# Kernel optimization log

Hardware: AMD Instinct MI355X
Metric: run time of the kernel (lower is better)

The kernel has to match this reference:

```python
import jax, jax.numpy as jnp
import numpy as np


def _conv1d(x, w, b):
    # x: [N, C_in, L], w: [C_out, C_in, K], padding=1 (SAME for K=3)
    y = jax.lax.conv_general_dilated(
        x, w, window_strides=(1,), padding=[(1, 1)],
        dimension_numbers=('NCH', 'OIH', 'NCH'))
    return y + b[None, :, None]


def _pharse_shift(I, r):
    # Faithful vectorized form of the original scalar loop:
    #   New[i, 0, j] = I[i, j % r, j // r];  all other output channels stay zero.
    a, b, c = I.shape
    row0 = jnp.transpose(I[:, :r, :], (0, 2, 1)).reshape(a, c * r)  # interleave channels
    New = jnp.zeros((a, b // r, c * r), dtype=I.dtype)
    return New.at[:, 0, :].set(row0)


def setup_inputs() -> dict:
    key = jax.random.key(0)
    k1, k2, k3, k4, k5 = jax.random.split(key, 5)
    B, C, L = 32, 64, 16384
    x = jax.random.normal(k1, (B, C, L), dtype=jnp.float32)
    # Conv1d(channels, channels, 3) params, PyTorch-style uniform init scale
    s1 = 1.0 / np.sqrt(C * 3)
    w1 = jax.random.uniform(k2, (C, C, 3), minval=-s1, maxval=s1, dtype=jnp.float32)
    b1 = jax.random.uniform(k3, (C,), minval=-s1, maxval=s1, dtype=jnp.float32)
    # Conv1d(channels, 4, 3) params (up_block22)
    w2 = jax.random.uniform(k4, (4, C, 3), minval=-s1, maxval=s1, dtype=jnp.float32)
    b2 = jax.random.uniform(k5, (4,), minval=-s1, maxval=s1, dtype=jnp.float32)
    return {"x": x, "w1": w1, "b1": b1, "w2": w2, "b2": b2, "sc": 4}


def reference(x, w1, b1, w2, b2, sc):
    assert sc in (2, 4)
    h = jax.nn.relu(_conv1d(x, w1, b1))   # up_block1: Conv1d(C,C,3)+ReLU
    h = jax.nn.relu(_conv1d(h, w2, b2))   # up_block22: Conv1d(C,4,3)+ReLU  [B,4,L]
    return _pharse_shift(h, sc)           # [B, 4//sc, L*sc]
```

## Files before the change

### kernel.cpp

```cpp
#include <hip/hip_runtime.h>


#define CC 64
#define LL 16384
#define NBATCH 32
#define TL 128
#define XROWS 146
#define PITCH 128

typedef short short8 __attribute__((ext_vector_type(8)));
typedef float f32x4 __attribute__((ext_vector_type(4)));

__device__ __forceinline__ unsigned short f2bf(float f) {
    unsigned u = __builtin_bit_cast(unsigned, f);
    u = (u + 0x7FFFu + ((u >> 16) & 1u)) >> 16;
    return (unsigned short)u;
}

__global__ void repack_weights(const float* __restrict__ w1,
                               const float* __restrict__ w2,
                               unsigned short* __restrict__ wp) {
    int i = blockIdx.x * 256 + threadIdx.x;
    if (i < 12288) {
        int kk = i >> 12;
        int rem = i & 4095;
        int co = rem >> 6;
        int ci = rem & 63;
        wp[i] = f2bf(w1[(co * 64 + ci) * 3 + kk]);
    }
    if (i < 3072) {
        int kk = i >> 10;
        int rem = i & 1023;
        int oc = rem >> 6;
        int ci = rem & 63;
        float v = (oc < 4) ? w2[(oc * 64 + ci) * 3 + kk] : 0.0f;
        wp[12288 + i] = f2bf(v);
    }
}

__global__ __launch_bounds__(256, 4)
void fused_upsample_mfma(const float* __restrict__ x,
                         const float* __restrict__ b1,
                         const float* __restrict__ b2,
                         const unsigned short* __restrict__ wp,
                         float* __restrict__ out) {
    __shared__ __align__(16) char lds[(148 + 144) * PITCH];
    char* const xs = lds;
    char* const hs = lds + 148 * PITCH;

    const int t    = blockIdx.x;
    const int bb   = blockIdx.y;
    const int tid  = threadIdx.x;
    const int lane = tid & 63;
    const int wave = tid >> 6;
    const int lr   = lane & 15;
    const int lg   = lane >> 4;

    {
        const int c   = tid & 15;
        const int cg  = tid >> 4;
        const int ci0 = cg * 4;
        const long xbase = (long)(bb * CC + ci0) * LL;
        #pragma unroll
        for (int it = 0; it < 10; ++it) {
            int row = it * 16 + c;
            if (row < XROWS) {
                int gx = t * TL - 2 + row;
                bool ok = (unsigned)gx < (unsigned)LL;
                float v0 = ok ? x[xbase + gx]          : 0.f;
                float v1 = ok ? x[xbase + LL + gx]     : 0.f;
                float v2 = ok ? x[xbase + 2 * LL + gx] : 0.f;
                float v3 = ok ? x[xbase + 3 * LL + gx] : 0.f;
                unsigned lo = (unsigned)f2bf(v0) | ((unsigned)f2bf(v1) << 16);
                unsigned hi = (unsigned)f2bf(v2) | ((unsigned)f2bf(v3) << 16);
                int byte = (row * PITCH + ci0 * 2) ^ ((row & 7) << 4);
                *(uint2*)(xs + byte) = make_uint2(lo, hi);
            }
        }
    }
    __syncthreads();

    {
        short8 A1[3][2];
        #pragma unroll
        for (int k = 0; k < 3; ++k)
            #pragma unroll
            for (int kc = 0; kc < 2; ++kc)
                A1[k][kc] = *(const short8*)(wp + ((k * 64 + wave * 16 + lr) * 64 + kc * 32 + lg * 8));

        const f32x4 bias1 = *(const f32x4*)(b1 + wave * 16 + lg * 4);

        #pragma unroll 1
        for (int i = 0; i < 9; ++i) {
            f32x4 acc = {0.f, 0.f, 0.f, 0.f};
            #pragma unroll
            for (int k = 0; k < 3; ++k) {
                int row = 16 * i + lr + k;
                #pragma unroll
                for (int kc = 0; kc < 2; ++kc) {
                    int byte = (row * PITCH + kc * 64 + lg * 16) ^ ((row & 7) << 4);
                    short8 Bf = *(const short8*)(xs + byte);
                    acc = __builtin_amdgcn_mfma_f32_16x16x32_bf16(A1[k][kc], Bf, acc, 0, 0, 0);
                }
            }
            int p  = 16 * i - 1 + lr;
            int hp = t * TL + p;
            bool inr = (unsigned)hp < (unsigned)LL;
            float r0 = inr ? fmaxf(acc[0] + bias1[0], 0.f) : 0.f;
            float r1 = inr ? fmaxf(acc[1] + bias1[1], 0.f) : 0.f;
            float r2 = inr ? fmaxf(acc[2] + bias1[2], 0.f) : 0.f;
            float r3 = inr ? fmaxf(acc[3] + bias1[3], 0.f) : 0.f;
            unsigned lo = (unsigned)f2bf(r0) | ((unsigned)f2bf(r1) << 16);
            unsigned hi = (unsigned)f2bf(r2) | ((unsigned)f2bf(r3) << 16);
            int hrow = 16 * i + lr;
            int byte = (hrow * PITCH + wave * 32 + lg * 8) ^ ((hrow & 7) << 4);
            *(uint2*)(hs + byte) = make_uint2(lo, hi);
        }
    }
    __syncthreads();

    {
        short8 A2[3][2];
        #pragma unroll
        for (int k = 0; k < 3; ++k)
            #pragma unroll
            for (int kc = 0; kc < 2; ++kc)
                A2[k][kc] = *(const short8*)(wp + 12288 + ((k * 16 + lr) * 64 + kc * 32 + lg * 8));

        const f32x4 bias2 = *(const f32x4*)(b2);

        #pragma unroll
        for (int s = 0; s < 2; ++s) {
            int p0 = 16 * (wave * 2 + s);
            f32x4 acc = {0.f, 0.f, 0.f, 0.f};
            #pragma unroll
            for (int k = 0; k < 3; ++k) {
                int row = p0 + lr + k;
                #pragma unroll
                for (int kc = 0; kc < 2; ++kc) {
                    int byte = (row * PITCH + kc * 64 + lg * 16) ^ ((row & 7) << 4);
                    short8 Bf = *(const short8*)(hs + byte);
                    acc = __builtin_amdgcn_mfma_f32_16x16x32_bf16(A2[k][kc], Bf, acc, 0, 0, 0);
                }
            }
            if (lane < 16) {
                f32x4 o;
                o[0] = fmaxf(acc[0] + bias2[0], 0.f);
                o[1] = fmaxf(acc[1] + bias2[1], 0.f);
                o[2] = fmaxf(acc[2] + bias2[2], 0.f);
                o[3] = fmaxf(acc[3] + bias2[3], 0.f);
                *(f32x4*)(out + (long)bb * (LL * 4) + (t * TL + p0 + lane) * 4) = o;
            }
        }
    }
}

extern "C" void kernel_launch(void* const* d_in, const int* in_sizes, int n_in,
                              void* d_out, int out_size, void* d_ws, size_t ws_size,
                              hipStream_t stream) {
    const float* x  = (const float*)d_in[0];
    const float* w1 = (const float*)d_in[1];
    const float* b1 = (const float*)d_in[2];
    const float* w2 = (const float*)d_in[3];
    const float* b2 = (const float*)d_in[4];
    float* out = (float*)d_out;
    unsigned short* wp = (unsigned short*)d_ws;

    repack_weights<<<48, 256, 0, stream>>>(w1, w2, wp);
    dim3 grid(LL / TL, NBATCH);
    fused_upsample_mfma<<<grid, 256, 0, stream>>>(x, b1, b2, wp, out);
}
```

Baseline: 64.11 us.

## Process four tiles per block with register-prefetched input and reorganized wave work split

Each block now loops over four consecutive L-tiles. It prefetches the next tile's x values into registers while the current tile's MFMA convolutions run, then writes them to LDS after the first barrier. Waves are re-split so each wave computes two output-channel groups over half the position chunks, sharing B fragments across two MFMAs. Biases are folded into the accumulator init, and bf16 conversion now uses the library intrinsic. This amortizes weight loads and hides global-load latency, at the cost of more registers (launch bounds lowered to 3), an extra barrier per tile, and a grid four times smaller.

```diff
diff --git a/kernel.cpp b/kernel.cpp
--- a/kernel.cpp
+++ b/kernel.cpp
@@ -1,20 +1,22 @@
 #include <hip/hip_runtime.h>
+#include <hip/hip_bf16.h>
 
 
 #define CC 64
 #define LL 16384
 #define NBATCH 32
 #define TL 128
+#define NT 4
 #define XROWS 146
 #define PITCH 128
 
 typedef short short8 __attribute__((ext_vector_type(8)));
 typedef float f32x4 __attribute__((ext_vector_type(4)));
 
-__device__ __forceinline__ unsigned short f2bf(float f) {
-    unsigned u = __builtin_bit_cast(unsigned, f);
-    u = (u + 0x7FFFu + ((u >> 16) & 1u)) >> 16;
-    return (unsigned short)u;
+__device__ __forceinline__ unsigned pk2(float a, float b) {
+    unsigned short lo = __builtin_bit_cast(unsigned short, __float2bfloat16(a));
+    unsigned short hi = __builtin_bit_cast(unsigned short, __float2bfloat16(b));
+    return (unsigned)lo | ((unsigned)hi << 16);
 }
 
 __global__ void repack_weights(const float* __restrict__ w1,
@@ -26,7 +28,7 @@
         int rem = i & 4095;
         int co = rem >> 6;
         int ci = rem & 63;
-        wp[i] = f2bf(w1[(co * 64 + ci) * 3 + kk]);
+        wp[i] = __builtin_bit_cast(unsigned short, __float2bfloat16(w1[(co * 64 + ci) * 3 + kk]));
     }
     if (i < 3072) {
         int kk = i >> 10;
@@ -34,105 +36,130 @@
         int oc = rem >> 6;
         int ci = rem & 63;
         float v = (oc < 4) ? w2[(oc * 64 + ci) * 3 + kk] : 0.0f;
-        wp[12288 + i] = f2bf(v);
-    }
-}
-
-__global__ __launch_bounds__(256, 4)
+        wp[12288 + i] = __builtin_bit_cast(unsigned short, __float2bfloat16(v));
+    }
+}
+
+__global__ __launch_bounds__(256, 3)
 void fused_upsample_mfma(const float* __restrict__ x,
                          const float* __restrict__ b1,
                          const float* __restrict__ b2,
                          const unsigned short* __restrict__ wp,
                          float* __restrict__ out) {
-    __shared__ __align__(16) char lds[(148 + 144) * PITCH];
+    __shared__ __align__(16) char lds[(XROWS + 144) * PITCH];
     char* const xs = lds;
-    char* const hs = lds + 148 * PITCH;
-
-    const int t    = blockIdx.x;
+    char* const hs = lds + XROWS * PITCH;
+
+    const int t0   = blockIdx.x * NT;
     const int bb   = blockIdx.y;
     const int tid  = threadIdx.x;
     const int lane = tid & 63;
     const int wave = tid >> 6;
     const int lr   = lane & 15;
     const int lg   = lane >> 4;
-
-    {
-        const int c   = tid & 15;
-        const int cg  = tid >> 4;
-        const int ci0 = cg * 4;
-        const long xbase = (long)(bb * CC + ci0) * LL;
-        #pragma unroll
-        for (int it = 0; it < 10; ++it) {
-            int row = it * 16 + c;
-            if (row < XROWS) {
-                int gx = t * TL - 2 + row;
-                bool ok = (unsigned)gx < (unsigned)LL;
-                float v0 = ok ? x[xbase + gx]          : 0.f;
-                float v1 = ok ? x[xbase + LL + gx]     : 0.f;
-                float v2 = ok ? x[xbase + 2 * LL + gx] : 0.f;
-                float v3 = ok ? x[xbase + 3 * LL + gx] : 0.f;
-                unsigned lo = (unsigned)f2bf(v0) | ((unsigned)f2bf(v1) << 16);
-                unsigned hi = (unsigned)f2bf(v2) | ((unsigned)f2bf(v3) << 16);
-                int byte = (row * PITCH + ci0 * 2) ^ ((row & 7) << 4);
-                *(uint2*)(xs + byte) = make_uint2(lo, hi);
-            }
-        }
-    }
-    __syncthreads();
-
-    {
-        short8 A1[3][2];
+    const int c2   = wave & 1;
+    const int ph   = wave >> 1;
+
+    short8 A1[2][3][2];
+    f32x4 bias1[2];
+    #pragma unroll
+    for (int u = 0; u < 2; ++u) {
         #pragma unroll
         for (int k = 0; k < 3; ++k)
             #pragma unroll
             for (int kc = 0; kc < 2; ++kc)
-                A1[k][kc] = *(const short8*)(wp + ((k * 64 + wave * 16 + lr) * 64 + kc * 32 + lg * 8));
-
-        const f32x4 bias1 = *(const f32x4*)(b1 + wave * 16 + lg * 4);
-
-        #pragma unroll 1
-        for (int i = 0; i < 9; ++i) {
-            f32x4 acc = {0.f, 0.f, 0.f, 0.f};
+                A1[u][k][kc] = *(const short8*)(wp + ((k * 64 + (c2 * 2 + u) * 16 + lr) * 64 + kc * 32 + lg * 8));
+        bias1[u] = *(const f32x4*)(b1 + (c2 * 2 + u) * 16 + lg * 4);
+    }
+    short8 A2[3][2];
+    #pragma unroll
+    for (int k = 0; k < 3; ++k)
+        #pragma unroll
+        for (int kc = 0; kc < 2; ++kc)
+            A2[k][kc] = *(const short8*)(wp + 12288 + ((k * 16 + lr) * 64 + kc * 32 + lg * 8));
+    const f32x4 bias2v = *(const f32x4*)(b2);
+    const f32x4 zero4 = {0.f, 0.f, 0.f, 0.f};
+    const f32x4 acc2init = (lg == 0) ? bias2v : zero4;
+
+    const int sc  = tid & 15;
+    const int scg = tid >> 4;
+    const long xbase = (long)(bb * CC + scg * 4) * LL;
+    float v[10][4];
+
+    auto issue = [&](int t) {
+        const int g0 = t * TL - 2;
+        #pragma unroll
+        for (int it = 0; it < 10; ++it) {
+            int row = it * 16 + sc;
+            int gx = g0 + row;
+            bool ok = (row < XROWS) && ((unsigned)gx < (unsigned)LL);
             #pragma unroll
-            for (int k = 0; k < 3; ++k) {
-                int row = 16 * i + lr + k;
+            for (int u = 0; u < 4; ++u)
+                v[it][u] = ok ? x[xbase + (long)u * LL + gx] : 0.f;
+        }
+    };
+    auto write_xs = [&]() {
+        #pragma unroll
+        for (int it = 0; it < 10; ++it) {
+            int row = it * 16 + sc;
+            if (row < XROWS) {
+                unsigned lo = pk2(v[it][0], v[it][1]);
+                unsigned hi = pk2(v[it][2], v[it][3]);
+                int byte = (row * PITCH + scg * 8) ^ ((row & 7) << 4);
+                *(uint2*)(xs + byte) = make_uint2(lo, hi);
+            }
+        }
+    };
+
+    issue(t0);
+    write_xs();
+    __syncthreads();
+
+    for (int j = 0; j < NT; ++j) {
+        const int t = t0 + j;
+        if (j + 1 < NT) issue(t + 1);
+
+        #pragma unroll
+        for (int ii = 0; ii < 5; ++ii) {
+            int i = ph * 5 + ii;
+            if (i < 9) {
+                f32x4 acc0 = bias1[0];
+                f32x4 acc1 = bias1[1];
                 #pragma unroll
-                for (int kc = 0; kc < 2; ++kc) {
-                    int byte = (row * PITCH + kc * 64 + lg * 16) ^ ((row & 7) << 4);
-                    short8 Bf = *(const short8*)(xs + byte);
-                    acc = __builtin_amdgcn_mfma_f32_16x16x32_bf16(A1[k][kc], Bf, acc, 0, 0, 0);
+                for (int k = 0; k < 3; ++k) {
+                    int row = 16 * i + lr + k;
+                    #pragma unroll
+                    for (int kc = 0; kc < 2; ++kc) {
+                        int byte = (row * PITCH + kc * 64 + lg * 16) ^ ((row & 7) << 4);
+                        short8 Bf = *(const short8*)(xs + byte);
+                        acc0 = __builtin_amdgcn_mfma_f32_16x16x32_bf16(A1[0][k][kc], Bf, acc0, 0, 0, 0);
+                        acc1 = __builtin_amdgcn_mfma_f32_16x16x32_bf16(A1[1][k][kc], Bf, acc1, 0, 0, 0);
+                    }
                 }
-            }
-            int p  = 16 * i - 1 + lr;
-            int hp = t * TL + p;
-            bool inr = (unsigned)hp < (unsigned)LL;
-            float r0 = inr ? fmaxf(acc[0] + bias1[0], 0.f) : 0.f;
-            float r1 = inr ? fmaxf(acc[1] + bias1[1], 0.f) : 0.f;
-            float r2 = inr ? fmaxf(acc[2] + bias1[2], 0.f) : 0.f;
-            float r3 = inr ? fmaxf(acc[3] + bias1[3], 0.f) : 0.f;
-            unsigned lo = (unsigned)f2bf(r0) | ((unsigned)f2bf(r1) << 16);
-            unsigned hi = (unsigned)f2bf(r2) | ((unsigned)f2bf(r3) << 16);
-            int hrow = 16 * i + lr;
-            int byte = (hrow * PITCH + wave * 32 + lg * 8) ^ ((hrow & 7) << 4);
-            *(uint2*)(hs + byte) = make_uint2(lo, hi);
-        }
-    }
-    __syncthreads();
-
-    {
-        short8 A2[3][2];
-        #pragma unroll
-        for (int k = 0; k < 3; ++k)
-            #pragma unroll
-            for (int kc = 0; kc < 2; ++kc)
-                A2[k][kc] = *(const short8*)(wp + 12288 + ((k * 16 + lr) * 64 + kc * 32 + lg * 8));
-
-        const f32x4 bias2 = *(const f32x4*)(b2);
+                int p  = 16 * i - 1 + lr;
+                int hp = t * TL + p;
+                bool inr = (unsigned)hp < (unsigned)LL;
+                int hrow = 16 * i + lr;
+                #pragma unroll
+                for (int u = 0; u < 2; ++u) {
+                    f32x4 a = u ? acc1 : acc0;
+                    float r0 = inr ? fmaxf(a[0], 0.f) : 0.f;
+                    float r1 = inr ? fmaxf(a[1], 0.f) : 0.f;
+                    float r2 = inr ? fmaxf(a[2], 0.f) : 0.f;
+                    float r3 = inr ? fmaxf(a[3], 0.f) : 0.f;
+                    int byte = (hrow * PITCH + (c2 * 2 + u) * 32 + lg * 8) ^ ((hrow & 7) << 4);
+                    *(uint2*)(hs + byte) = make_uint2(pk2(r0, r1), pk2(r2, r3));
+                }
+            }
+        }
+        __syncthreads();
+
+        if (j + 1 < NT) write_xs();
 
         #pragma unroll
         for (int s = 0; s < 2; ++s) {
             int p0 = 16 * (wave * 2 + s);
-            f32x4 acc = {0.f, 0.f, 0.f, 0.f};
+            f32x4 acc = acc2init;
             #pragma unroll
             for (int k = 0; k < 3; ++k) {
                 int row = p0 + lr + k;
@@ -145,13 +172,14 @@
             }
             if (lane < 16) {
                 f32x4 o;
-                o[0] = fmaxf(acc[0] + bias2[0], 0.f);
-                o[1] = fmaxf(acc[1] + bias2[1], 0.f);
-                o[2] = fmaxf(acc[2] + bias2[2], 0.f);
-                o[3] = fmaxf(acc[3] + bias2[3], 0.f);
+                o[0] = fmaxf(acc[0], 0.f);
+                o[1] = fmaxf(acc[1], 0.f);
+                o[2] = fmaxf(acc[2], 0.f);
+                o[3] = fmaxf(acc[3], 0.f);
                 *(f32x4*)(out + (long)bb * (LL * 4) + (t * TL + p0 + lane) * 4) = o;
             }
         }
+        __syncthreads();
     }
 }
 
@@ -167,6 +195,6 @@
     unsigned short* wp = (unsigned short*)d_ws;
 
     repack_weights<<<48, 256, 0, stream>>>(w1, w2, wp);
-    dim3 grid(LL / TL, NBATCH);
+    dim3 grid(LL / (TL * NT), NBATCH);
     fused_upsample_mfma<<<grid, 256, 0, stream>>>(x, b1, b2, wp, out);
 }
```

Result: slower. 158.2 us (+146.8%).
